# Optimization experiments

Hardware: AMD Instinct MI355X
Metric: run time of the kernel (lower is better)

## Reference

```python
import jax, jax.numpy as jnp
import numpy as np

H = 2048           # hidden size
IN_F = 64          # in_features
OUT_F = 3          # out_features
NEG_SLOPE = 0.01   # LeakyReLU default


def setup_inputs() -> dict:
    key = jax.random.key(0)
    ks = jax.random.split(key, 11)
    N = 32768
    return {
        "p": jax.random.normal(ks[0], (N, IN_F), dtype=jnp.float32),
        "init_w": jax.random.normal(ks[1], (H, IN_F), dtype=jnp.float32) * 0.05,
        "init_b": jax.random.normal(ks[2], (H,), dtype=jnp.float32) * 0.05,
        "w1": jax.random.normal(ks[3], (H, H), dtype=jnp.float32) * 0.02,
        "b1": jax.random.normal(ks[4], (H,), dtype=jnp.float32) * 0.02,
        "w2": jax.random.normal(ks[5], (H, H), dtype=jnp.float32) * 0.02,
        "b2": jax.random.normal(ks[6], (H,), dtype=jnp.float32) * 0.02,
        "w3": jax.random.normal(ks[7], (H, H), dtype=jnp.float32) * 0.02,
        "b3": jax.random.normal(ks[8], (H,), dtype=jnp.float32) * 0.02,
        "out_w": jax.random.normal(ks[9], (OUT_F, H), dtype=jnp.float32) * 0.05,
        "out_b": jax.random.normal(ks[10], (OUT_F,), dtype=jnp.float32) * 0.05,
    }


def _leaky_relu(x):
    return jnp.where(x > 0, x, NEG_SLOPE * x)


def reference(p, init_w, init_b, w1, b1, w2, b2, w3, b3, out_w, out_b):
    # eval mode: StructuredDropout with eval_size=None -> plain init linear
    flat = p.reshape(-1, p.shape[-1])                      # [N, IN_F]
    x = flat @ init_w.T + init_b                           # [N, H]
    # upper-triangular mask (in==out, backflow=0 -> diagonal=0)
    mask = jnp.triu(jnp.ones((H, H), dtype=bool))
    # hidden TriangleLinear layers; flip = (i % 2 == 1)
    for W, b, flip in ((w1, b1, False), (w2, b2, True), (w3, b3, False)):
        y = _leaky_relu(x) @ jnp.where(mask, W, 0.0).T + b  # [N, H]
        x = y[..., ::-1] if flip else y
    x = _leaky_relu(x)
    out = x @ out_w.T + out_b                              # [N, OUT_F]
    return out.reshape(p.shape[:-1] + (OUT_F,))
```

## Files before the change

kernel.cpp:

```cpp
#include <hip/hip_runtime.h>
#include <hip/hip_bf16.h>

#define NEG 0.01f

using f32x4  = __attribute__((ext_vector_type(4))) float;
using bf16x8 = __attribute__((ext_vector_type(8))) short;

__device__ __forceinline__ unsigned short f2b(float f) {
  union { float f; unsigned int u; } v; v.f = f;
  unsigned int r = (v.u + 0x7fffu + ((v.u >> 16) & 1u)) >> 16;
  return (unsigned short)r;
}
__device__ __forceinline__ float b2f(unsigned int bits) {
  union { unsigned int u; float f; } v; v.u = bits << 16;
  return v.f;
}

__device__ __forceinline__ void gload16(const unsigned short* g, unsigned short* l) {
  __builtin_amdgcn_global_load_lds(
      (const __attribute__((address_space(1))) unsigned int*)g,
      (__attribute__((address_space(3))) unsigned int*)l, 16, 0, 0);
}

__global__ void k_cvt(const float* __restrict__ in, unsigned short* __restrict__ out, int n4) {
  int i = blockIdx.x * blockDim.x + threadIdx.x;
  int stride = gridDim.x * blockDim.x;
  for (; i < n4; i += stride) {
    float4 v = reinterpret_cast<const float4*>(in)[i];
    ushort4 o;
    o.x = f2b(v.x); o.y = f2b(v.y); o.z = f2b(v.z); o.w = f2b(v.w);
    reinterpret_cast<ushort4*>(out)[i] = o;
  }
}

__global__ void k_cvt_tri(const float* __restrict__ W, unsigned short* __restrict__ out, int anti) {
  const int H = 2048;
  int i = blockIdx.x;
  const float* wr = W + (size_t)i * H;
  unsigned short* orow = out + (size_t)i * H;
  if (!anti) {
    for (int j = threadIdx.x; j < H; j += blockDim.x) {
      float v = (j >= i) ? wr[j] : 0.f;
      orow[j] = f2b(v);
    }
  } else {
    for (int k = threadIdx.x; k < H; k += blockDim.x) {
      int j = H - 1 - k;
      float v = (j >= i) ? wr[j] : 0.f;
      orow[k] = f2b(v);
    }
  }
}

__launch_bounds__(512, 2)
__global__ void k_gemm8(const unsigned short* __restrict__ A, int lda,
                        const unsigned short* __restrict__ B, int ldb,
                        const float* __restrict__ bias,
                        unsigned short* __restrict__ C, int ldc,
                        int K, int mode) {
  extern __shared__ unsigned short lds[];
  const int tid = threadIdx.x;
  const int w   = tid >> 6;
  const int l   = tid & 63;

  const int nwg = gridDim.x;
  const int q8  = nwg >> 3;
  const int L   = blockIdx.x;
  const int logical = (L & 7) * q8 + (L >> 3);
  const int by = logical >> 3;
  const int bx = (logical + by) & 7;
  const int brow = by * 256;
  const int bcol = bx * 256;

  int kstart = 0, kend = K;
  if (mode == 1) kstart = bcol;
  else if (mode == 2) kend = K - bcol;
  const int nt = (kend - kstart) >> 6;

  const int wm = w >> 2;
  const int wn = w & 3;

  f32x4 acc[8][4];
#pragma unroll
  for (int i = 0; i < 8; i++)
#pragma unroll
    for (int j = 0; j < 4; j++) acc[i][j] = (f32x4){0.f, 0.f, 0.f, 0.f};

  const int srow  = l >> 2;
  const int sperm = ((l & 3) - ((l >> 3) & 3)) & 3;
  const unsigned short* Asrc = A + (size_t)(brow + w * 16 + srow) * lda + sperm * 8;
  const unsigned short* Bsrc = B + (size_t)(bcol + w * 16 + srow) * ldb + sperm * 8;
  const int rdoff = (l & 15) * 64 + ((((l >> 4) + ((l >> 1) & 7)) & 3) << 4);

  auto ldsAt = [&](int byteoff) -> unsigned short* {
    return (unsigned short*)((char*)lds + byteoff);
  };
  auto stage_tile = [&](int tk, int bb) {
    const int kc = kstart + (tk << 6);
#pragma unroll
    for (int half = 0; half < 2; half++) {
#pragma unroll
      for (int qq = 0; qq < 2; qq++) {
        gload16(Asrc + (size_t)(half * 128) * lda + kc + qq * 32,
                ldsAt(bb * 65536 + half * 16384 + (w * 2 + qq) * 1024));
        gload16(Bsrc + (size_t)(half * 128) * ldb + kc + qq * 32,
                ldsAt(bb * 65536 + 32768 + half * 16384 + (w * 2 + qq) * 1024));
      }
    }
  };

  stage_tile(0, 0);
  if (nt > 1) stage_tile(1, 1);

  const int AbaseW = wm * 16384;
  const int BbaseW = 32768 + (wn >> 1) * 16384 + (wn & 1) * 8192;

  for (int t = 0; t < nt; t++) {
    const int bb = t & 1;
    const int Ab = bb * 65536 + AbaseW;
    const int Bb = bb * 65536 + BbaseW;
    if (t + 1 < nt) asm volatile("s_waitcnt vmcnt(8)" ::: "memory");
    else            asm volatile("s_waitcnt vmcnt(0)" ::: "memory");
    __builtin_amdgcn_s_barrier();
    asm volatile("" ::: "memory");

    bf16x8 aR[4][2], bR[2][2];
#pragma unroll
    for (int Q = 0; Q < 4; Q++) {
      const int mh = Q >> 1, nh = Q & 1;
      if (nh == 0) {
#pragma unroll
        for (int ii = 0; ii < 4; ii++)
#pragma unroll
          for (int kk = 0; kk < 2; kk++)
            aR[ii][kk] = *(const bf16x8*)((char*)lds + Ab + ((mh * 4 + ii) * 2 + kk) * 1024 + rdoff);
      }
#pragma unroll
      for (int jj = 0; jj < 2; jj++)
#pragma unroll
        for (int kk = 0; kk < 2; kk++)
          bR[jj][kk] = *(const bf16x8*)((char*)lds + Bb + ((nh * 2 + jj) * 2 + kk) * 1024 + rdoff);

      __builtin_amdgcn_s_setprio(1);
#pragma unroll
      for (int ii = 0; ii < 4; ii++)
#pragma unroll
        for (int jj = 0; jj < 2; jj++) {
          acc[mh * 4 + ii][nh * 2 + jj] = __builtin_amdgcn_mfma_f32_16x16x32_bf16(
              aR[ii][0], bR[jj][0], acc[mh * 4 + ii][nh * 2 + jj], 0, 0, 0);
          acc[mh * 4 + ii][nh * 2 + jj] = __builtin_amdgcn_mfma_f32_16x16x32_bf16(
              aR[ii][1], bR[jj][1], acc[mh * 4 + ii][nh * 2 + jj], 0, 0, 0);
        }
      __builtin_amdgcn_s_setprio(0);
      if (Q < 3) __builtin_amdgcn_s_barrier();
    }
    asm volatile("s_waitcnt lgkmcnt(0)" ::: "memory");
    __builtin_amdgcn_s_barrier();
    asm volatile("" ::: "memory");
    if (t + 2 < nt) stage_tile(t + 2, bb);
  }

  const int orow0 = brow + wm * 128 + ((l >> 4) << 2);
  const int ocol0 = bcol + wn * 64 + (l & 15);
#pragma unroll
  for (int j = 0; j < 4; j++) {
    const int col = ocol0 + j * 16;
    const float bv = bias[col];
#pragma unroll
    for (int i = 0; i < 8; i++) {
#pragma unroll
      for (int r = 0; r < 4; r++) {
        const int row = orow0 + i * 16 + r;
        float v = acc[i][j][r] + bv;
        v = v > 0.f ? v : NEG * v;
        C[(size_t)row * ldc + col] = f2b(v);
      }
    }
  }
}

__global__ void k_out(const unsigned short* __restrict__ A,
                      const float* __restrict__ ow, const float* __restrict__ ob,
                      float* __restrict__ out) {
  const int H = 2048;
  int w = threadIdx.x >> 6, lane = threadIdx.x & 63;
  size_t n = (size_t)blockIdx.x * 4 + w;
  const unsigned short* a = A + n * H;
  float s0 = 0.f, s1 = 0.f, s2 = 0.f;
  for (int h0 = lane * 8; h0 < H; h0 += 512) {
    uint4 u = *reinterpret_cast<const uint4*>(&a[h0]);
    unsigned int uu[4] = {u.x, u.y, u.z, u.w};
#pragma unroll
    for (int q = 0; q < 4; q++) {
      int h = h0 + q * 2;
      float x0 = b2f(uu[q] & 0xffffu);
      float x1 = b2f(uu[q] >> 16);
      s0 += x0 * ow[h]         + x1 * ow[h + 1];
      s1 += x0 * ow[H + h]     + x1 * ow[H + h + 1];
      s2 += x0 * ow[2 * H + h] + x1 * ow[2 * H + h + 1];
    }
  }
#pragma unroll
  for (int off = 32; off > 0; off >>= 1) {
    s0 += __shfl_down(s0, off);
    s1 += __shfl_down(s1, off);
    s2 += __shfl_down(s2, off);
  }
  if (lane == 0) {
    out[n * 3 + 0] = s0 + ob[0];
    out[n * 3 + 1] = s1 + ob[1];
    out[n * 3 + 2] = s2 + ob[2];
  }
}

extern "C" void kernel_launch(void* const* d_in, const int* in_sizes, int n_in,
                              void* d_out, int out_size, void* d_ws, size_t ws_size,
                              hipStream_t stream) {
  const int N = 32768, H = 2048, INF_ = 64;
  const float* p      = (const float*)d_in[0];
  const float* init_w = (const float*)d_in[1];
  const float* init_b = (const float*)d_in[2];
  const float* w1     = (const float*)d_in[3];
  const float* b1     = (const float*)d_in[4];
  const float* w2     = (const float*)d_in[5];
  const float* b2     = (const float*)d_in[6];
  const float* w3     = (const float*)d_in[7];
  const float* b3     = (const float*)d_in[8];
  const float* ow     = (const float*)d_in[9];
  const float* ob     = (const float*)d_in[10];

  hipFuncSetAttribute((const void*)k_gemm8,
                      hipFuncAttributeMaxDynamicSharedMemorySize, 131072);

  char* wsb = (char*)d_ws;
  size_t off = 0;
  auto alloc = [&](size_t bytes) -> char* {
    char* q = wsb + off;
    off += (bytes + 255) & ~(size_t)255;
    return q;
  };
  unsigned short* pb  = (unsigned short*)alloc((size_t)N * INF_ * 2);
  unsigned short* iwb = (unsigned short*)alloc((size_t)H * INF_ * 2);
  unsigned short* w1m = (unsigned short*)alloc((size_t)H * H * 2);
  unsigned short* w2m = (unsigned short*)alloc((size_t)H * H * 2);
  unsigned short* w3m = (unsigned short*)alloc((size_t)H * H * 2);

  size_t remain = (ws_size > off) ? (ws_size - off) : 0;
  long long ncll = (long long)(remain / ((size_t)H * 2 * 2));
  int Nc = (int)((ncll / 256) * 256);
  if (Nc > N) Nc = N;
  if (Nc < 256) return;

  unsigned short* bufA = (unsigned short*)(wsb + off);
  unsigned short* bufB = bufA + (size_t)Nc * H;

  k_cvt<<<2048, 256, 0, stream>>>(p, pb, N * INF_ / 4);
  k_cvt<<<32,   256, 0, stream>>>(init_w, iwb, H * INF_ / 4);
  k_cvt_tri<<<H, 256, 0, stream>>>(w1, w1m, 0);
  k_cvt_tri<<<H, 256, 0, stream>>>(w2, w2m, 0);
  k_cvt_tri<<<H, 256, 0, stream>>>(w3, w3m, 1);

  for (int n0 = 0; n0 < N; n0 += Nc) {
    int nc = (N - n0 < Nc) ? (N - n0) : Nc;
    int nblk = (nc / 256) * (H / 256);
    k_gemm8<<<nblk, 512, 131072, stream>>>(pb + (size_t)n0 * INF_, INF_, iwb, INF_,
                                           init_b, bufA, H, INF_, 0);
    k_gemm8<<<nblk, 512, 131072, stream>>>(bufA, H, w1m, H, b1, bufB, H, H, 1);
    k_gemm8<<<nblk, 512, 131072, stream>>>(bufB, H, w2m, H, b2, bufA, H, H, 1);
    k_gemm8<<<nblk, 512, 131072, stream>>>(bufA, H, w3m, H, b3, bufB, H, H, 2);
    k_out<<<nc / 4, 256, 0, stream>>>(bufB, ow, ob, (float*)d_out + (size_t)n0 * 3);
  }
}
```

Baseline: 903.2 us.

## Use persistent GEMM grid with paired triangular tiles for load balance

Replaces the one-block-per-tile launch with a fixed grid of 256 persistent blocks. Each block loops over pairs of column tiles (pr, 7-pr) so that the short-K and long-K triangular tiles are balanced per work item. The per-k-step quadrant loop is also reordered to reuse loaded B fragments and to overlap the next tile's staging with the last MFMA quadrant. This costs extra loop overhead and assumes 256 blocks (two per CU) fill the device.

```diff
diff --git a/kernel.cpp b/kernel.cpp
--- a/kernel.cpp
+++ b/kernel.cpp
@@ -57,123 +57,162 @@
                         const unsigned short* __restrict__ B, int ldb,
                         const float* __restrict__ bias,
                         unsigned short* __restrict__ C, int ldc,
-                        int K, int mode) {
+                        int K, int mode, int NB) {
   extern __shared__ unsigned short lds[];
   const int tid = threadIdx.x;
   const int w   = tid >> 6;
   const int l   = tid & 63;
 
-  const int nwg = gridDim.x;
-  const int q8  = nwg >> 3;
-  const int L   = blockIdx.x;
-  const int logical = (L & 7) * q8 + (L >> 3);
-  const int by = logical >> 3;
-  const int bx = (logical + by) & 7;
-  const int brow = by * 256;
-  const int bcol = bx * 256;
-
-  int kstart = 0, kend = K;
-  if (mode == 1) kstart = bcol;
-  else if (mode == 2) kend = K - bcol;
-  const int nt = (kend - kstart) >> 6;
-
-  const int wm = w >> 2;
-  const int wn = w & 3;
-
-  f32x4 acc[8][4];
-#pragma unroll
-  for (int i = 0; i < 8; i++)
-#pragma unroll
-    for (int j = 0; j < 4; j++) acc[i][j] = (f32x4){0.f, 0.f, 0.f, 0.f};
+  const int G = gridDim.x;
+  const int P = blockIdx.x;
+  const int b = (P & 7) * (G >> 3) + (P >> 3);
 
   const int srow  = l >> 2;
   const int sperm = ((l & 3) - ((l >> 3) & 3)) & 3;
-  const unsigned short* Asrc = A + (size_t)(brow + w * 16 + srow) * lda + sperm * 8;
-  const unsigned short* Bsrc = B + (size_t)(bcol + w * 16 + srow) * ldb + sperm * 8;
   const int rdoff = (l & 15) * 64 + ((((l >> 4) + ((l >> 1) & 7)) & 3) << 4);
-
-  auto ldsAt = [&](int byteoff) -> unsigned short* {
-    return (unsigned short*)((char*)lds + byteoff);
-  };
-  auto stage_tile = [&](int tk, int bb) {
-    const int kc = kstart + (tk << 6);
-#pragma unroll
-    for (int half = 0; half < 2; half++) {
-#pragma unroll
-      for (int qq = 0; qq < 2; qq++) {
-        gload16(Asrc + (size_t)(half * 128) * lda + kc + qq * 32,
-                ldsAt(bb * 65536 + half * 16384 + (w * 2 + qq) * 1024));
-        gload16(Bsrc + (size_t)(half * 128) * ldb + kc + qq * 32,
-                ldsAt(bb * 65536 + 32768 + half * 16384 + (w * 2 + qq) * 1024));
-      }
-    }
-  };
-
-  stage_tile(0, 0);
-  if (nt > 1) stage_tile(1, 1);
-
+  const int wm = w >> 2, wn = w & 3;
   const int AbaseW = wm * 16384;
   const int BbaseW = 32768 + (wn >> 1) * 16384 + (wn & 1) * 8192;
 
-  for (int t = 0; t < nt; t++) {
-    const int bb = t & 1;
-    const int Ab = bb * 65536 + AbaseW;
-    const int Bb = bb * 65536 + BbaseW;
-    if (t + 1 < nt) asm volatile("s_waitcnt vmcnt(8)" ::: "memory");
-    else            asm volatile("s_waitcnt vmcnt(0)" ::: "memory");
-    __builtin_amdgcn_s_barrier();
-    asm volatile("" ::: "memory");
-
-    bf16x8 aR[4][2], bR[2][2];
-#pragma unroll
-    for (int Q = 0; Q < 4; Q++) {
-      const int mh = Q >> 1, nh = Q & 1;
-      if (nh == 0) {
-#pragma unroll
-        for (int ii = 0; ii < 4; ii++)
-#pragma unroll
-          for (int kk = 0; kk < 2; kk++)
-            aR[ii][kk] = *(const bf16x8*)((char*)lds + Ab + ((mh * 4 + ii) * 2 + kk) * 1024 + rdoff);
+  const int npairs = NB * 4;
+#pragma unroll 1
+  for (int p = b; p < npairs; p += G) {
+    const int by = p >> 2;
+    const int pr = p & 3;
+#pragma unroll 1
+    for (int side = 0; side < 2; side++) {
+      const int bx = side ? (7 - pr) : pr;
+      const int brow = by * 256;
+      const int bcol = bx * 256;
+      int kstart = 0, kend = K;
+      if (mode == 1) kstart = bcol;
+      else if (mode == 2) kend = K - bcol;
+      const int nt = (kend - kstart) >> 6;
+
+      const unsigned short* Asrc = A + (size_t)(brow + w * 16 + srow) * lda + sperm * 8;
+      const unsigned short* Bsrc = B + (size_t)(bcol + w * 16 + srow) * ldb + sperm * 8;
+
+      auto stage_tile = [&](int tk, int bb) {
+        const int kc = kstart + (tk << 6);
+#pragma unroll
+        for (int half = 0; half < 2; half++) {
+#pragma unroll
+          for (int qq = 0; qq < 2; qq++) {
+            gload16(Asrc + (size_t)(half * 128) * lda + kc + qq * 32,
+                    (unsigned short*)((char*)lds + bb * 65536 + half * 16384 + (w * 2 + qq) * 1024));
+            gload16(Bsrc + (size_t)(half * 128) * ldb + kc + qq * 32,
+                    (unsigned short*)((char*)lds + bb * 65536 + 32768 + half * 16384 + (w * 2 + qq) * 1024));
+          }
+        }
+      };
+
+      f32x4 acc[8][4];
+#pragma unroll
+      for (int i = 0; i < 8; i++)
+#pragma unroll
+        for (int j = 0; j < 4; j++) acc[i][j] = (f32x4){0.f, 0.f, 0.f, 0.f};
+
+      stage_tile(0, 0);
+      if (nt > 1) stage_tile(1, 1);
+
+#pragma unroll 1
+      for (int t = 0; t < nt; t++) {
+        const int bb = t & 1;
+        const char* Ab = (const char*)lds + bb * 65536 + AbaseW;
+        const char* Bb = (const char*)lds + bb * 65536 + BbaseW;
+        if (t + 1 < nt) asm volatile("s_waitcnt vmcnt(8)" ::: "memory");
+        else            asm volatile("s_waitcnt vmcnt(0)" ::: "memory");
+        __builtin_amdgcn_s_barrier();
+        asm volatile("" ::: "memory");
+
+        bf16x8 aR[4][2], bRa[2][2], bRb[2][2];
+#pragma unroll
+        for (int ii = 0; ii < 4; ii++)
+#pragma unroll
+          for (int kk = 0; kk < 2; kk++)
+            aR[ii][kk] = *(const bf16x8*)(Ab + (ii * 2 + kk) * 1024 + rdoff);
+#pragma unroll
+        for (int jj = 0; jj < 2; jj++)
+#pragma unroll
+          for (int kk = 0; kk < 2; kk++)
+            bRa[jj][kk] = *(const bf16x8*)(Bb + (jj * 2 + kk) * 1024 + rdoff);
+        __builtin_amdgcn_s_setprio(1);
+#pragma unroll
+        for (int ii = 0; ii < 4; ii++)
+#pragma unroll
+          for (int jj = 0; jj < 2; jj++) {
+            acc[ii][jj] = __builtin_amdgcn_mfma_f32_16x16x32_bf16(aR[ii][0], bRa[jj][0], acc[ii][jj], 0, 0, 0);
+            acc[ii][jj] = __builtin_amdgcn_mfma_f32_16x16x32_bf16(aR[ii][1], bRa[jj][1], acc[ii][jj], 0, 0, 0);
+          }
+        __builtin_amdgcn_s_setprio(0);
+        __builtin_amdgcn_s_barrier();
+        asm volatile("" ::: "memory");
+#pragma unroll
+        for (int jj = 0; jj < 2; jj++)
+#pragma unroll
+          for (int kk = 0; kk < 2; kk++)
+            bRb[jj][kk] = *(const bf16x8*)(Bb + ((2 + jj) * 2 + kk) * 1024 + rdoff);
+        __builtin_amdgcn_s_setprio(1);
+#pragma unroll
+        for (int ii = 0; ii < 4; ii++)
+#pragma unroll
+          for (int jj = 0; jj < 2; jj++) {
+            acc[ii][2 + jj] = __builtin_amdgcn_mfma_f32_16x16x32_bf16(aR[ii][0], bRb[jj][0], acc[ii][2 + jj], 0, 0, 0);
+            acc[ii][2 + jj] = __builtin_amdgcn_mfma_f32_16x16x32_bf16(aR[ii][1], bRb[jj][1], acc[ii][2 + jj], 0, 0, 0);
+          }
+        __builtin_amdgcn_s_setprio(0);
+        __builtin_amdgcn_s_barrier();
+        asm volatile("" ::: "memory");
+#pragma unroll
+        for (int ii = 0; ii < 4; ii++)
+#pragma unroll
+          for (int kk = 0; kk < 2; kk++)
+            aR[ii][kk] = *(const bf16x8*)(Ab + ((4 + ii) * 2 + kk) * 1024 + rdoff);
+#pragma unroll
+        for (int jj = 0; jj < 2; jj++)
+#pragma unroll
+          for (int kk = 0; kk < 2; kk++)
+            bRa[jj][kk] = *(const bf16x8*)(Bb + (jj * 2 + kk) * 1024 + rdoff);
+        __builtin_amdgcn_s_setprio(1);
+#pragma unroll
+        for (int ii = 0; ii < 4; ii++)
+#pragma unroll
+          for (int jj = 0; jj < 2; jj++) {
+            acc[4 + ii][2 + jj] = __builtin_amdgcn_mfma_f32_16x16x32_bf16(aR[ii][0], bRb[jj][0], acc[4 + ii][2 + jj], 0, 0, 0);
+            acc[4 + ii][2 + jj] = __builtin_amdgcn_mfma_f32_16x16x32_bf16(aR[ii][1], bRb[jj][1], acc[4 + ii][2 + jj], 0, 0, 0);
+          }
+        __builtin_amdgcn_s_setprio(0);
+        asm volatile("s_waitcnt lgkmcnt(0)" ::: "memory");
+        __builtin_amdgcn_s_barrier();
+        asm volatile("" ::: "memory");
+        if (t + 2 < nt) stage_tile(t + 2, bb);
+        __builtin_amdgcn_s_setprio(1);
+#pragma unroll
+        for (int ii = 0; ii < 4; ii++)
+#pragma unroll
+          for (int jj = 0; jj < 2; jj++) {
+            acc[4 + ii][jj] = __builtin_amdgcn_mfma_f32_16x16x32_bf16(aR[ii][0], bRa[jj][0], acc[4 + ii][jj], 0, 0, 0);
+            acc[4 + ii][jj] = __builtin_amdgcn_mfma_f32_16x16x32_bf16(aR[ii][1], bRa[jj][1], acc[4 + ii][jj], 0, 0, 0);
+          }
+        __builtin_amdgcn_s_setprio(0);
       }
-#pragma unroll
-      for (int jj = 0; jj < 2; jj++)
-#pragma unroll
-        for (int kk = 0; kk < 2; kk++)
-          bR[jj][kk] = *(const bf16x8*)((char*)lds + Bb + ((nh * 2 + jj) * 2 + kk) * 1024 + rdoff);
-
-      __builtin_amdgcn_s_setprio(1);
-#pragma unroll
-      for (int ii = 0; ii < 4; ii++)
-#pragma unroll
-        for (int jj = 0; jj < 2; jj++) {
-          acc[mh * 4 + ii][nh * 2 + jj] = __builtin_amdgcn_mfma_f32_16x16x32_bf16(
-              aR[ii][0], bR[jj][0], acc[mh * 4 + ii][nh * 2 + jj], 0, 0, 0);
-          acc[mh * 4 + ii][nh * 2 + jj] = __builtin_amdgcn_mfma_f32_16x16x32_bf16(
-              aR[ii][1], bR[jj][1], acc[mh * 4 + ii][nh * 2 + jj], 0, 0, 0);
+
+      const int orow0 = brow + wm * 128 + ((l >> 4) << 2);
+      const int ocol0 = bcol + wn * 64 + (l & 15);
+#pragma unroll
+      for (int j = 0; j < 4; j++) {
+        const int col = ocol0 + j * 16;
+        const float bv = bias[col];
+#pragma unroll
+        for (int i = 0; i < 8; i++) {
+#pragma unroll
+          for (int r = 0; r < 4; r++) {
+            const int row = orow0 + i * 16 + r;
+            float v = acc[i][j][r] + bv;
+            v = v > 0.f ? v : NEG * v;
+            C[(size_t)row * ldc + col] = f2b(v);
+          }
         }
-      __builtin_amdgcn_s_setprio(0);
-      if (Q < 3) __builtin_amdgcn_s_barrier();
-    }
-    asm volatile("s_waitcnt lgkmcnt(0)" ::: "memory");
-    __builtin_amdgcn_s_barrier();
-    asm volatile("" ::: "memory");
-    if (t + 2 < nt) stage_tile(t + 2, bb);
-  }
-
-  const int orow0 = brow + wm * 128 + ((l >> 4) << 2);
-  const int ocol0 = bcol + wn * 64 + (l & 15);
-#pragma unroll
-  for (int j = 0; j < 4; j++) {
-    const int col = ocol0 + j * 16;
-    const float bv = bias[col];
-#pragma unroll
-    for (int i = 0; i < 8; i++) {
-#pragma unroll
-      for (int r = 0; r < 4; r++) {
-        const int row = orow0 + i * 16 + r;
-        float v = acc[i][j][r] + bv;
-        v = v > 0.f ? v : NEG * v;
-        C[(size_t)row * ldc + col] = f2b(v);
       }
     }
   }
@@ -262,12 +301,12 @@
 
   for (int n0 = 0; n0 < N; n0 += Nc) {
     int nc = (N - n0 < Nc) ? (N - n0) : Nc;
-    int nblk = (nc / 256) * (H / 256);
-    k_gemm8<<<nblk, 512, 131072, stream>>>(pb + (size_t)n0 * INF_, INF_, iwb, INF_,
-                                           init_b, bufA, H, INF_, 0);
-    k_gemm8<<<nblk, 512, 131072, stream>>>(bufA, H, w1m, H, b1, bufB, H, H, 1);
-    k_gemm8<<<nblk, 512, 131072, stream>>>(bufB, H, w2m, H, b2, bufA, H, H, 1);
-    k_gemm8<<<nblk, 512, 131072, stream>>>(bufA, H, w3m, H, b3, bufB, H, H, 2);
+    int NB = nc / 256;
+    k_gemm8<<<256, 512, 131072, stream>>>(pb + (size_t)n0 * INF_, INF_, iwb, INF_,
+                                          init_b, bufA, H, INF_, 0, NB);
+    k_gemm8<<<256, 512, 131072, stream>>>(bufA, H, w1m, H, b1, bufB, H, H, 1, NB);
+    k_gemm8<<<256, 512, 131072, stream>>>(bufB, H, w2m, H, b2, bufA, H, H, 1, NB);
+    k_gemm8<<<256, 512, 131072, stream>>>(bufA, H, w3m, H, b3, bufB, H, H, 2, NB);
     k_out<<<nc / 4, 256, 0, stream>>>(bufB, ow, ob, (float*)d_out + (size_t)n0 * 3);
   }
 }
```

After: 953.7 us. +5.6%, slower.
